# Kernel tuning notes

Measured on AMD Instinct MI355X. Metric: run time of the kernel, lower is better.

The kernel has to match this reference:

```python
import jax, jax.numpy as jnp
import numpy as np

N = 1_048_576      # flattened batch (forward reshapes to (-1, 4))
Q_DIM = 4
HIDDEN = 64
DC = Q_DIM // 2    # q_dim_changed = 2
NUM_LO = (DC * DC - DC) // 2  # = 1
SLOPE = 0.01       # torch leaky_relu default negative slope


def setup_inputs() -> dict:
    key = jax.random.key(0)
    ks = jax.random.split(key, 9)
    def lin(kw, kb, fan_out, fan_in):
        bound = 1.0 / np.sqrt(fan_in)
        W = jax.random.uniform(kw, (fan_out, fan_in), jnp.float32, -bound, bound)
        b = jax.random.uniform(kb, (fan_out,), jnp.float32, -bound, bound)
        return W, b
    x = jax.random.normal(ks[0], (N, Q_DIM), jnp.float32)
    W1, b1 = lin(ks[1], ks[2], HIDDEN, Q_DIM)
    W2, b2 = lin(ks[3], ks[4], HIDDEN, HIDDEN)
    W_Ld, b_Ld = lin(ks[5], ks[6], DC, HIDDEN)
    W_Lo, b_Lo = lin(ks[7], ks[8], NUM_LO, HIDDEN)
    return {"x": x, "W1": W1, "b1": b1, "W2": W2, "b2": b2,
            "W_Ld": W_Ld, "b_Ld": b_Ld, "W_Lo": W_Lo, "b_Lo": b_Lo}


def reference(x, W1, b1, W2, b2, W_Ld, b_Ld, W_Lo, b_Lo):
    q = x.reshape(-1, Q_DIM)                      # (n, 4)
    n = q.shape[0]
    h1 = jax.nn.leaky_relu(q @ W1.T + b1, SLOPE)  # (n, 64)
    h2 = jax.nn.leaky_relu(h1 @ W2.T + b2, SLOPE) # (n, 64); dropout is eval-mode identity
    Ld = jax.nn.softplus(h2 @ W_Ld.T + b_Ld)      # (n, 2) positive diagonal
    Lo = h2 @ W_Lo.T + b_Lo                       # (n, 1) strictly-lower entries
    rows, cols = jnp.tril_indices(DC, -1)         # strictly lower triangle, row-major
    diag = jnp.arange(DC)
    L = jnp.zeros((n, DC, DC), dtype=q.dtype)
    L = L.at[:, rows, cols].set(Lo)               # scatter Lo (matches torch boolean-mask fill order)
    L = L.at[:, diag, diag].set(Ld)               # diag_embed(Ld)
    H = jnp.einsum('nij,nkj->nik', L, L) + 1e-9 * jnp.eye(DC, dtype=q.dtype)
    return H
```

## Files before the change

### kernel.cpp

```cpp
#include <hip/hip_runtime.h>


typedef __attribute__((ext_vector_type(8))) short bf16x8;
typedef __attribute__((ext_vector_type(4))) float f32x4;
typedef __attribute__((ext_vector_type(2))) float f32x2;

#define BLOCK_THREADS 256
#define GRID_BLOCKS   1024

__device__ __forceinline__ float lrelu(float a) {
    return fmaxf(a, 0.01f * a);
}

__device__ __forceinline__ f32x2 lrelu2(f32x2 a) {
    return __builtin_elementwise_max(a, a * 0.01f);
}

__device__ __forceinline__ float softplus(float v) {
    return fmaxf(v, 0.0f) + log1pf(expf(-fabsf(v)));
}

__device__ __forceinline__ unsigned cvt_pk_bf16(float lo, float hi) {
    unsigned r;
    asm("v_cvt_pk_bf16_f32 %0, %1, %2" : "=v"(r) : "v"(lo), "v"(hi));
    return r;
}

__global__ __launch_bounds__(BLOCK_THREADS) void dln_mfma(
    const float* __restrict__ x,
    const float* __restrict__ W1,  const float* __restrict__ b1,
    const float* __restrict__ W2,  const float* __restrict__ b2,
    const float* __restrict__ WLd, const float* __restrict__ bLd,
    const float* __restrict__ WLo, const float* __restrict__ bLo,
    float* __restrict__ out,
    int iters, int iter_stride)
{
    __shared__ __align__(16) unsigned short h1s[4][8][64][8];

    const int tid  = threadIdx.x;
    const int lane = tid & 63;
    const int wv   = tid >> 6;
    const int quad = lane >> 4;
    const int c    = lane & 15;

    int row = blockIdx.x * BLOCK_THREADS + tid;
    float4 qnext = ((const float4*)x)[row];

    bf16x8 afrag[4][2];
    f32x4 wld0[4], wld1[4], wlo[4], b2v[4];
#pragma unroll
    for (int mt = 0; mt < 4; ++mt) {
        const float* wr = W2 + (16 * mt + c) * 64 + 8 * quad;
#pragma unroll
        for (int s = 0; s < 2; ++s) {
            const float4 f0 = *(const float4*)(wr + 32 * s);
            const float4 f1 = *(const float4*)(wr + 32 * s + 4);
            uint4 u;
            u.x = cvt_pk_bf16(f0.x, f0.y);
            u.y = cvt_pk_bf16(f0.z, f0.w);
            u.z = cvt_pk_bf16(f1.x, f1.y);
            u.w = cvt_pk_bf16(f1.z, f1.w);
            afrag[mt][s] = __builtin_bit_cast(bf16x8, u);
        }
        const int nb = 16 * mt + 4 * quad;
        wld0[mt] = *(const f32x4*)(WLd + nb);
        wld1[mt] = *(const f32x4*)(WLd + 64 + nb);
        wlo[mt]  = *(const f32x4*)(WLo + nb);
        b2v[mt]  = *(const f32x4*)(b2 + nb);
    }
    const float bld0 = bLd[0];
    const float bld1 = bLd[1];
    const float blo0 = bLo[0];

    for (int itr = 0; itr < iters; ++itr) {
        const float4 qv = qnext;
        const int row_cur = row;
        row += iter_stride;
        if (itr + 1 < iters)
            qnext = ((const float4*)x)[row];

#pragma unroll
        for (int ch = 0; ch < 8; ++ch) {
            unsigned up[4];
#pragma unroll
            for (int p = 0; p < 4; ++p) {
                float h[2];
#pragma unroll
                for (int e = 0; e < 2; ++e) {
                    const int j = ch * 8 + p * 2 + e;
                    float a = b1[j];
                    a = fmaf(qv.x, W1[4 * j + 0], a);
                    a = fmaf(qv.y, W1[4 * j + 1], a);
                    a = fmaf(qv.z, W1[4 * j + 2], a);
                    a = fmaf(qv.w, W1[4 * j + 3], a);
                    h[e] = lrelu(a);
                }
                up[p] = cvt_pk_bf16(h[0], h[1]);
            }
            *(uint4*)&h1s[wv][ch][lane][0] = make_uint4(up[0], up[1], up[2], up[3]);
        }

        float sld0 = 0.0f, sld1 = 0.0f, slo = 0.0f;
#pragma unroll
        for (int it = 0; it < 4; ++it) {
            const bf16x8 bf0 = *(const bf16x8*)&h1s[wv][quad][it * 16 + c][0];
            const bf16x8 bf1 = *(const bf16x8*)&h1s[wv][4 + quad][it * 16 + c][0];

            f32x2 pld0 = {0.0f, 0.0f}, pld1 = {0.0f, 0.0f}, plo = {0.0f, 0.0f};
#pragma unroll
            for (int mt = 0; mt < 4; ++mt) {
                f32x4 acc = b2v[mt];
                acc = __builtin_amdgcn_mfma_f32_16x16x32_bf16(afrag[mt][0], bf0, acc, 0, 0, 0);
                acc = __builtin_amdgcn_mfma_f32_16x16x32_bf16(afrag[mt][1], bf1, acc, 0, 0, 0);
                const f32x2 hlo = lrelu2((f32x2){acc[0], acc[1]});
                const f32x2 hhi = lrelu2((f32x2){acc[2], acc[3]});
                pld0 = __builtin_elementwise_fma(hlo, (f32x2){wld0[mt][0], wld0[mt][1]}, pld0);
                pld0 = __builtin_elementwise_fma(hhi, (f32x2){wld0[mt][2], wld0[mt][3]}, pld0);
                pld1 = __builtin_elementwise_fma(hlo, (f32x2){wld1[mt][0], wld1[mt][1]}, pld1);
                pld1 = __builtin_elementwise_fma(hhi, (f32x2){wld1[mt][2], wld1[mt][3]}, pld1);
                plo  = __builtin_elementwise_fma(hlo, (f32x2){wlo[mt][0],  wlo[mt][1]},  plo);
                plo  = __builtin_elementwise_fma(hhi, (f32x2){wlo[mt][2],  wlo[mt][3]},  plo);
            }
            float r0 = pld0[0] + pld0[1];
            float r1 = pld1[0] + pld1[1];
            float r2 = plo[0]  + plo[1];
            r0 += __shfl_xor(r0, 16); r0 += __shfl_xor(r0, 32);
            r1 += __shfl_xor(r1, 16); r1 += __shfl_xor(r1, 32);
            r2 += __shfl_xor(r2, 16); r2 += __shfl_xor(r2, 32);
            if (it == quad) { sld0 = r0; sld1 = r1; slo = r2; }
        }

        {
            const float ld0 = softplus(sld0 + bld0);
            const float ld1 = softplus(sld1 + bld1);
            const float lo  = slo + blo0;
            float4 o;
            o.x = fmaf(ld0, ld0, 1e-9f);
            o.y = ld0 * lo;
            o.z = o.y;
            o.w = fmaf(lo, lo, fmaf(ld1, ld1, 1e-9f));
            reinterpret_cast<float4*>(out)[row_cur] = o;
        }
    }
}

__global__ __launch_bounds__(256) void dln_tail(
    const float* __restrict__ x,
    const float* __restrict__ W1,  const float* __restrict__ b1,
    const float* __restrict__ W2,  const float* __restrict__ b2,
    const float* __restrict__ WLd, const float* __restrict__ bLd,
    const float* __restrict__ WLo, const float* __restrict__ bLo,
    float* __restrict__ out, int row0, int nrows)
{
    const int row = row0 + blockIdx.x * 256 + threadIdx.x;
    if (row >= nrows) return;
    const float4 qv = reinterpret_cast<const float4*>(x)[row];
    float h1[64];
#pragma unroll
    for (int j = 0; j < 64; ++j) {
        float a = b1[j];
        a = fmaf(qv.x, W1[4 * j + 0], a);
        a = fmaf(qv.y, W1[4 * j + 1], a);
        a = fmaf(qv.z, W1[4 * j + 2], a);
        a = fmaf(qv.w, W1[4 * j + 3], a);
        h1[j] = lrelu(a);
    }
    float ld0 = bLd[0], ld1 = bLd[1], lo = bLo[0];
#pragma unroll 4
    for (int j = 0; j < 64; ++j) {
        float a0 = b2[j], a1 = 0.0f;
        const float* w = W2 + 64 * j;
#pragma unroll
        for (int k = 0; k < 64; k += 2) {
            a0 = fmaf(h1[k],     w[k],     a0);
            a1 = fmaf(h1[k + 1], w[k + 1], a1);
        }
        const float a = lrelu(a0 + a1);
        ld0 = fmaf(a, WLd[j],      ld0);
        ld1 = fmaf(a, WLd[64 + j], ld1);
        lo  = fmaf(a, WLo[j],      lo);
    }
    ld0 = softplus(ld0);
    ld1 = softplus(ld1);
    float4 o;
    o.x = fmaf(ld0, ld0, 1e-9f);
    o.y = ld0 * lo;
    o.z = o.y;
    o.w = fmaf(lo, lo, fmaf(ld1, ld1, 1e-9f));
    reinterpret_cast<float4*>(out)[row] = o;
}

extern "C" void kernel_launch(void* const* d_in, const int* in_sizes, int n_in,
                              void* d_out, int out_size, void* d_ws, size_t ws_size,
                              hipStream_t stream)
{
    const float* x   = (const float*)d_in[0];
    const float* W1  = (const float*)d_in[1];
    const float* b1  = (const float*)d_in[2];
    const float* W2  = (const float*)d_in[3];
    const float* b2  = (const float*)d_in[4];
    const float* WLd = (const float*)d_in[5];
    const float* bLd = (const float*)d_in[6];
    const float* WLo = (const float*)d_in[7];
    const float* bLo = (const float*)d_in[8];
    float* out = (float*)d_out;

    const int nrows  = in_sizes[0] / 4;
    const int stripe = GRID_BLOCKS * BLOCK_THREADS;
    const int iters  = nrows / stripe;
    const int nfull  = iters * stripe;
    const int rem    = nrows - nfull;

    if (iters > 0)
        dln_mfma<<<GRID_BLOCKS, BLOCK_THREADS, 0, stream>>>(
            x, W1, b1, W2, b2, WLd, bLd, WLo, bLo, out, iters, stripe);
    if (rem > 0)
        dln_tail<<<(rem + 255) / 256, 256, 0, stream>>>(
            x, W1, b1, W2, b2, WLd, bLd, WLo, bLo, out, nfull, nrows);
}
```

Before: 120.6 us.

## Compute first layer with split-bf16 MFMA and drop the LDS staging

Moves the 4→64 first layer from scalar FMAs onto MFMA. W1, the bias and x are split into hi/lo bf16 pairs and three MFMAs per tile recover near-fp32 accuracy, with the bias folded in through a constant-one input column. The layer-1 output now arrives directly in the register layout needed as the B operand of layer 2, so the shared-memory write/read round trip is removed. Row assignment changes to contiguous 256-row groups per block. This cuts VALU work and LDS traffic at the cost of extra MFMA issues, and x is now loaded redundantly across the four quads of each wave.

```diff
diff --git a/kernel.cpp b/kernel.cpp
--- a/kernel.cpp
+++ b/kernel.cpp
@@ -5,8 +5,9 @@
 typedef __attribute__((ext_vector_type(4))) float f32x4;
 typedef __attribute__((ext_vector_type(2))) float f32x2;
 
-#define BLOCK_THREADS 256
-#define GRID_BLOCKS   1024
+#define BLOCK_THREADS  256
+#define GRID_BLOCKS    1024
+#define ROWS_PER_GROUP 256
 
 __device__ __forceinline__ float lrelu(float a) {
     return fmaxf(a, 0.01f * a);
@@ -24,6 +25,11 @@
     unsigned r;
     asm("v_cvt_pk_bf16_f32 %0, %1, %2" : "=v"(r) : "v"(lo), "v"(hi));
     return r;
+}
+
+__device__ __forceinline__ float lo_of(float v, unsigned pk, bool hi_half) {
+    const float h = __uint_as_float(hi_half ? (pk & 0xFFFF0000u) : (pk << 16));
+    return v - h;
 }
 
 __global__ __launch_bounds__(BLOCK_THREADS) void dln_mfma(
@@ -32,19 +38,32 @@
     const float* __restrict__ W2,  const float* __restrict__ b2,
     const float* __restrict__ WLd, const float* __restrict__ bLd,
     const float* __restrict__ WLo, const float* __restrict__ bLo,
-    float* __restrict__ out,
-    int iters, int iter_stride)
+    float* __restrict__ out, int ngroups)
 {
-    __shared__ __align__(16) unsigned short h1s[4][8][64][8];
-
     const int tid  = threadIdx.x;
     const int lane = tid & 63;
     const int wv   = tid >> 6;
     const int quad = lane >> 4;
     const int c    = lane & 15;
 
-    int row = blockIdx.x * BLOCK_THREADS + tid;
-    float4 qnext = ((const float4*)x)[row];
+    bf16x8 a1hi[4], a1lo[4];
+#pragma unroll
+    for (int mt = 0; mt < 4; ++mt) {
+        const int nu = 32 * (mt >> 1) + 8 * (c >> 2) + 4 * (mt & 1) + (c & 3);
+        const float4 w = *(const float4*)(W1 + 4 * nu);
+        const float bb = b1[nu];
+        const unsigned h01 = cvt_pk_bf16(w.x, w.y);
+        const unsigned h23 = cvt_pk_bf16(w.z, w.w);
+        const unsigned hb  = cvt_pk_bf16(bb, 0.0f);
+        const unsigned l01 = cvt_pk_bf16(lo_of(w.x, h01, false), lo_of(w.y, h01, true));
+        const unsigned l23 = cvt_pk_bf16(lo_of(w.z, h23, false), lo_of(w.w, h23, true));
+        const unsigned lb  = cvt_pk_bf16(lo_of(bb, hb, false), 0.0f);
+        const uint4 z  = make_uint4(0u, 0u, 0u, 0u);
+        const uint4 uh = (quad == 0) ? make_uint4(h01, h23, hb, 0u) : z;
+        const uint4 ul = (quad == 0) ? make_uint4(l01, l23, lb, 0u) : z;
+        a1hi[mt] = __builtin_bit_cast(bf16x8, uh);
+        a1lo[mt] = __builtin_bit_cast(bf16x8, ul);
+    }
 
     bf16x8 afrag[4][2];
     f32x4 wld0[4], wld1[4], wlo[4], b2v[4];
@@ -72,39 +91,50 @@
     const float bld1 = bLd[1];
     const float blo0 = bLo[0];
 
-    for (int itr = 0; itr < iters; ++itr) {
-        const float4 qv = qnext;
-        const int row_cur = row;
-        row += iter_stride;
-        if (itr + 1 < iters)
-            qnext = ((const float4*)x)[row];
-
-#pragma unroll
-        for (int ch = 0; ch < 8; ++ch) {
-            unsigned up[4];
-#pragma unroll
-            for (int p = 0; p < 4; ++p) {
-                float h[2];
-#pragma unroll
-                for (int e = 0; e < 2; ++e) {
-                    const int j = ch * 8 + p * 2 + e;
-                    float a = b1[j];
-                    a = fmaf(qv.x, W1[4 * j + 0], a);
-                    a = fmaf(qv.y, W1[4 * j + 1], a);
-                    a = fmaf(qv.z, W1[4 * j + 2], a);
-                    a = fmaf(qv.w, W1[4 * j + 3], a);
-                    h[e] = lrelu(a);
-                }
-                up[p] = cvt_pk_bf16(h[0], h[1]);
+    for (int grp = blockIdx.x; grp < ngroups; grp += gridDim.x) {
+        const int wbase = grp * ROWS_PER_GROUP + wv * 64;
+
+        float4 xv[4];
+#pragma unroll
+        for (int it = 0; it < 4; ++it)
+            xv[it] = ((const float4*)x)[wbase + it * 16 + c];
+
+        float sld0 = 0.0f, sld1 = 0.0f, slo = 0.0f;
+#pragma unroll
+        for (int it = 0; it < 4; ++it) {
+            const unsigned xh01 = cvt_pk_bf16(xv[it].x, xv[it].y);
+            const unsigned xh23 = cvt_pk_bf16(xv[it].z, xv[it].w);
+            const unsigned xl01 = cvt_pk_bf16(lo_of(xv[it].x, xh01, false),
+                                              lo_of(xv[it].y, xh01, true));
+            const unsigned xl23 = cvt_pk_bf16(lo_of(xv[it].z, xh23, false),
+                                              lo_of(xv[it].w, xh23, true));
+            const uint4 z  = make_uint4(0u, 0u, 0u, 0u);
+            const uint4 bh = (quad == 0) ? make_uint4(xh01, xh23, 0x00003F80u, 0u) : z;
+            const uint4 bl = (quad == 0) ? make_uint4(xl01, xl23, 0u, 0u) : z;
+            const bf16x8 bqh = __builtin_bit_cast(bf16x8, bh);
+            const bf16x8 bql = __builtin_bit_cast(bf16x8, bl);
+
+            f32x4 acc1[4];
+#pragma unroll
+            for (int mt = 0; mt < 4; ++mt) {
+                f32x4 a = (f32x4){0.0f, 0.0f, 0.0f, 0.0f};
+                a = __builtin_amdgcn_mfma_f32_16x16x32_bf16(a1hi[mt], bqh, a, 0, 0, 0);
+                a = __builtin_amdgcn_mfma_f32_16x16x32_bf16(a1hi[mt], bql, a, 0, 0, 0);
+                a = __builtin_amdgcn_mfma_f32_16x16x32_bf16(a1lo[mt], bqh, a, 0, 0, 0);
+                acc1[mt] = a;
             }
-            *(uint4*)&h1s[wv][ch][lane][0] = make_uint4(up[0], up[1], up[2], up[3]);
-        }
-
-        float sld0 = 0.0f, sld1 = 0.0f, slo = 0.0f;
-#pragma unroll
-        for (int it = 0; it < 4; ++it) {
-            const bf16x8 bf0 = *(const bf16x8*)&h1s[wv][quad][it * 16 + c][0];
-            const bf16x8 bf1 = *(const bf16x8*)&h1s[wv][4 + quad][it * 16 + c][0];
+
+            uint4 u0, u1;
+            u0.x = cvt_pk_bf16(lrelu(acc1[0][0]), lrelu(acc1[0][1]));
+            u0.y = cvt_pk_bf16(lrelu(acc1[0][2]), lrelu(acc1[0][3]));
+            u0.z = cvt_pk_bf16(lrelu(acc1[1][0]), lrelu(acc1[1][1]));
+            u0.w = cvt_pk_bf16(lrelu(acc1[1][2]), lrelu(acc1[1][3]));
+            u1.x = cvt_pk_bf16(lrelu(acc1[2][0]), lrelu(acc1[2][1]));
+            u1.y = cvt_pk_bf16(lrelu(acc1[2][2]), lrelu(acc1[2][3]));
+            u1.z = cvt_pk_bf16(lrelu(acc1[3][0]), lrelu(acc1[3][1]));
+            u1.w = cvt_pk_bf16(lrelu(acc1[3][2]), lrelu(acc1[3][3]));
+            const bf16x8 bf0 = __builtin_bit_cast(bf16x8, u0);
+            const bf16x8 bf1 = __builtin_bit_cast(bf16x8, u1);
 
             f32x2 pld0 = {0.0f, 0.0f}, pld1 = {0.0f, 0.0f}, plo = {0.0f, 0.0f};
 #pragma unroll
@@ -139,7 +169,7 @@
             o.y = ld0 * lo;
             o.z = o.y;
             o.w = fmaf(lo, lo, fmaf(ld1, ld1, 1e-9f));
-            reinterpret_cast<float4*>(out)[row_cur] = o;
+            reinterpret_cast<float4*>(out)[wbase + lane] = o;
         }
     }
 }
@@ -205,15 +235,16 @@
     const float* bLo = (const float*)d_in[8];
     float* out = (float*)d_out;
 
-    const int nrows  = in_sizes[0] / 4;
-    const int stripe = GRID_BLOCKS * BLOCK_THREADS;
-    const int iters  = nrows / stripe;
-    const int nfull  = iters * stripe;
-    const int rem    = nrows - nfull;
-
-    if (iters > 0)
-        dln_mfma<<<GRID_BLOCKS, BLOCK_THREADS, 0, stream>>>(
-            x, W1, b1, W2, b2, WLd, bLd, WLo, bLo, out, iters, stripe);
+    const int nrows   = in_sizes[0] / 4;
+    const int ngroups = nrows / ROWS_PER_GROUP;
+    const int nfull   = ngroups * ROWS_PER_GROUP;
+    const int rem     = nrows - nfull;
+
+    if (ngroups > 0) {
+        const int grid = (ngroups < GRID_BLOCKS) ? ngroups : GRID_BLOCKS;
+        dln_mfma<<<grid, BLOCK_THREADS, 0, stream>>>(
+            x, W1, b1, W2, b2, WLd, bLd, WLo, bLo, out, ngroups);
+    }
     if (rem > 0)
         dln_tail<<<(rem + 255) / 256, 256, 0, stream>>>(
             x, W1, b1, W2, b2, WLd, bLd, WLo, bLo, out, nfull, nrows);
```

Result: slower. 133.9 us (+11.0%).

## Compute output head with split-bf16 MFMA and permute W2 rows for fragment reuse

Applied to the files above, without the earlier changes.

Replaces the per-lane FMA head projection and cross-lane shuffle reductions with an extra MFMA. Layer-2 activations are repacked into bf16 B-fragments, and W2 rows are permuted so the accumulator layout matches the next MFMA's input. The head weights are split into hi and lo bf16 parts to keep near-fp32 accuracy. The launch also switches to a 1280-block grid-stride loop over 256-row groups. The cost is that layer-2 activations are now rounded to bf16 before the head, which adds precision error.

```diff
diff --git a/kernel.cpp b/kernel.cpp
--- a/kernel.cpp
+++ b/kernel.cpp
@@ -5,8 +5,9 @@
 typedef __attribute__((ext_vector_type(4))) float f32x4;
 typedef __attribute__((ext_vector_type(2))) float f32x2;
 
-#define BLOCK_THREADS 256
-#define GRID_BLOCKS   1024
+#define BLOCK_THREADS  256
+#define GRID_BLOCKS    1280
+#define ROWS_PER_GROUP 256
 
 __device__ __forceinline__ float lrelu(float a) {
     return fmaxf(a, 0.01f * a);
@@ -24,6 +25,11 @@
     unsigned r;
     asm("v_cvt_pk_bf16_f32 %0, %1, %2" : "=v"(r) : "v"(lo), "v"(hi));
     return r;
+}
+
+__device__ __forceinline__ float lo_of(float v, unsigned pk, bool hi_half) {
+    const float h = __uint_as_float(hi_half ? (pk & 0xFFFF0000u) : (pk << 16));
+    return v - h;
 }
 
 __global__ __launch_bounds__(BLOCK_THREADS) void dln_mfma(
@@ -32,8 +38,7 @@
     const float* __restrict__ W2,  const float* __restrict__ b2,
     const float* __restrict__ WLd, const float* __restrict__ bLd,
     const float* __restrict__ WLo, const float* __restrict__ bLo,
-    float* __restrict__ out,
-    int iters, int iter_stride)
+    float* __restrict__ out, int ngroups)
 {
     __shared__ __align__(16) unsigned short h1s[4][8][64][8];
 
@@ -43,14 +48,15 @@
     const int quad = lane >> 4;
     const int c    = lane & 15;
 
-    int row = blockIdx.x * BLOCK_THREADS + tid;
-    float4 qnext = ((const float4*)x)[row];
+    int grp = blockIdx.x;
+    float4 qnext = ((const float4*)x)[grp * ROWS_PER_GROUP + tid];
 
     bf16x8 afrag[4][2];
-    f32x4 wld0[4], wld1[4], wlo[4], b2v[4];
+    f32x4 b2v[4];
 #pragma unroll
     for (int mt = 0; mt < 4; ++mt) {
-        const float* wr = W2 + (16 * mt + c) * 64 + 8 * quad;
+        const int nu = 32 * (mt >> 1) + 8 * (c >> 2) + 4 * (mt & 1) + (c & 3);
+        const float* wr = W2 + nu * 64 + 8 * quad;
 #pragma unroll
         for (int s = 0; s < 2; ++s) {
             const float4 f0 = *(const float4*)(wr + 32 * s);
@@ -62,22 +68,45 @@
             u.w = cvt_pk_bf16(f1.z, f1.w);
             afrag[mt][s] = __builtin_bit_cast(bf16x8, u);
         }
-        const int nb = 16 * mt + 4 * quad;
-        wld0[mt] = *(const f32x4*)(WLd + nb);
-        wld1[mt] = *(const f32x4*)(WLd + 64 + nb);
-        wlo[mt]  = *(const f32x4*)(WLo + nb);
-        b2v[mt]  = *(const f32x4*)(b2 + nb);
+        b2v[mt] = *(const f32x4*)(b2 + 32 * (mt >> 1) + 4 * (mt & 1) + 8 * quad);
+    }
+
+    bf16x8 hA[2][2];
+    {
+        const float* hw = (c == 0) ? WLd : (c == 1) ? (WLd + 64) : WLo;
+#pragma unroll
+        for (int s = 0; s < 2; ++s) {
+            uint4 uh = make_uint4(0u, 0u, 0u, 0u);
+            uint4 ul = make_uint4(0u, 0u, 0u, 0u);
+            if (c < 3) {
+                const float* p = hw + 32 * s + 8 * quad;
+                const float4 f0 = *(const float4*)(p);
+                const float4 f1 = *(const float4*)(p + 4);
+                uh.x = cvt_pk_bf16(f0.x, f0.y);
+                uh.y = cvt_pk_bf16(f0.z, f0.w);
+                uh.z = cvt_pk_bf16(f1.x, f1.y);
+                uh.w = cvt_pk_bf16(f1.z, f1.w);
+                ul.x = cvt_pk_bf16(lo_of(f0.x, uh.x, false), lo_of(f0.y, uh.x, true));
+                ul.y = cvt_pk_bf16(lo_of(f0.z, uh.y, false), lo_of(f0.w, uh.y, true));
+                ul.z = cvt_pk_bf16(lo_of(f1.x, uh.z, false), lo_of(f1.y, uh.z, true));
+                ul.w = cvt_pk_bf16(lo_of(f1.z, uh.w, false), lo_of(f1.w, uh.w, true));
+            }
+            hA[s][0] = __builtin_bit_cast(bf16x8, uh);
+            hA[s][1] = __builtin_bit_cast(bf16x8, ul);
+        }
     }
     const float bld0 = bLd[0];
     const float bld1 = bLd[1];
     const float blo0 = bLo[0];
-
-    for (int itr = 0; itr < iters; ++itr) {
+    const f32x4 hinit = (quad == 0) ? (f32x4){bld0, bld1, blo0, 0.0f}
+                                    : (f32x4){0.0f, 0.0f, 0.0f, 0.0f};
+
+    for (; grp < ngroups; grp += (int)gridDim.x) {
         const float4 qv = qnext;
-        const int row_cur = row;
-        row += iter_stride;
-        if (itr + 1 < iters)
-            qnext = ((const float4*)x)[row];
+        const int gn = grp + (int)gridDim.x;
+        if (gn < ngroups)
+            qnext = ((const float4*)x)[gn * ROWS_PER_GROUP + tid];
+        const int wbase = grp * ROWS_PER_GROUP + wv * 64;
 
 #pragma unroll
         for (int ch = 0; ch < 8; ++ch) {
@@ -100,13 +129,12 @@
             *(uint4*)&h1s[wv][ch][lane][0] = make_uint4(up[0], up[1], up[2], up[3]);
         }
 
-        float sld0 = 0.0f, sld1 = 0.0f, slo = 0.0f;
 #pragma unroll
         for (int it = 0; it < 4; ++it) {
             const bf16x8 bf0 = *(const bf16x8*)&h1s[wv][quad][it * 16 + c][0];
             const bf16x8 bf1 = *(const bf16x8*)&h1s[wv][4 + quad][it * 16 + c][0];
 
-            f32x2 pld0 = {0.0f, 0.0f}, pld1 = {0.0f, 0.0f}, plo = {0.0f, 0.0f};
+            uint4 u0, u1;
 #pragma unroll
             for (int mt = 0; mt < 4; ++mt) {
                 f32x4 acc = b2v[mt];
@@ -114,32 +142,33 @@
                 acc = __builtin_amdgcn_mfma_f32_16x16x32_bf16(afrag[mt][1], bf1, acc, 0, 0, 0);
                 const f32x2 hlo = lrelu2((f32x2){acc[0], acc[1]});
                 const f32x2 hhi = lrelu2((f32x2){acc[2], acc[3]});
-                pld0 = __builtin_elementwise_fma(hlo, (f32x2){wld0[mt][0], wld0[mt][1]}, pld0);
-                pld0 = __builtin_elementwise_fma(hhi, (f32x2){wld0[mt][2], wld0[mt][3]}, pld0);
-                pld1 = __builtin_elementwise_fma(hlo, (f32x2){wld1[mt][0], wld1[mt][1]}, pld1);
-                pld1 = __builtin_elementwise_fma(hhi, (f32x2){wld1[mt][2], wld1[mt][3]}, pld1);
-                plo  = __builtin_elementwise_fma(hlo, (f32x2){wlo[mt][0],  wlo[mt][1]},  plo);
-                plo  = __builtin_elementwise_fma(hhi, (f32x2){wlo[mt][2],  wlo[mt][3]},  plo);
-            }
-            float r0 = pld0[0] + pld0[1];
-            float r1 = pld1[0] + pld1[1];
-            float r2 = plo[0]  + plo[1];
-            r0 += __shfl_xor(r0, 16); r0 += __shfl_xor(r0, 32);
-            r1 += __shfl_xor(r1, 16); r1 += __shfl_xor(r1, 32);
-            r2 += __shfl_xor(r2, 16); r2 += __shfl_xor(r2, 32);
-            if (it == quad) { sld0 = r0; sld1 = r1; slo = r2; }
-        }
-
-        {
-            const float ld0 = softplus(sld0 + bld0);
-            const float ld1 = softplus(sld1 + bld1);
-            const float lo  = slo + blo0;
-            float4 o;
-            o.x = fmaf(ld0, ld0, 1e-9f);
-            o.y = ld0 * lo;
-            o.z = o.y;
-            o.w = fmaf(lo, lo, fmaf(ld1, ld1, 1e-9f));
-            reinterpret_cast<float4*>(out)[row_cur] = o;
+                const unsigned pa = cvt_pk_bf16(hlo[0], hlo[1]);
+                const unsigned pb = cvt_pk_bf16(hhi[0], hhi[1]);
+                if (mt == 0)      { u0.x = pa; u0.y = pb; }
+                else if (mt == 1) { u0.z = pa; u0.w = pb; }
+                else if (mt == 2) { u1.x = pa; u1.y = pb; }
+                else              { u1.z = pa; u1.w = pb; }
+            }
+            const bf16x8 bh0 = __builtin_bit_cast(bf16x8, u0);
+            const bf16x8 bh1 = __builtin_bit_cast(bf16x8, u1);
+
+            f32x4 hacc = hinit;
+            hacc = __builtin_amdgcn_mfma_f32_16x16x32_bf16(hA[0][0], bh0, hacc, 0, 0, 0);
+            hacc = __builtin_amdgcn_mfma_f32_16x16x32_bf16(hA[0][1], bh0, hacc, 0, 0, 0);
+            hacc = __builtin_amdgcn_mfma_f32_16x16x32_bf16(hA[1][0], bh1, hacc, 0, 0, 0);
+            hacc = __builtin_amdgcn_mfma_f32_16x16x32_bf16(hA[1][1], bh1, hacc, 0, 0, 0);
+
+            if (quad == 0) {
+                const float ld0 = softplus(hacc[0]);
+                const float ld1 = softplus(hacc[1]);
+                const float lo  = hacc[2];
+                float4 o;
+                o.x = fmaf(ld0, ld0, 1e-9f);
+                o.y = ld0 * lo;
+                o.z = o.y;
+                o.w = fmaf(lo, lo, fmaf(ld1, ld1, 1e-9f));
+                reinterpret_cast<float4*>(out)[wbase + it * 16 + c] = o;
+            }
         }
     }
 }
@@ -205,15 +234,16 @@
     const float* bLo = (const float*)d_in[8];
     float* out = (float*)d_out;
 
-    const int nrows  = in_sizes[0] / 4;
-    const int stripe = GRID_BLOCKS * BLOCK_THREADS;
-    const int iters  = nrows / stripe;
-    const int nfull  = iters * stripe;
-    const int rem    = nrows - nfull;
-
-    if (iters > 0)
-        dln_mfma<<<GRID_BLOCKS, BLOCK_THREADS, 0, stream>>>(
-            x, W1, b1, W2, b2, WLd, bLd, WLo, bLo, out, iters, stripe);
+    const int nrows   = in_sizes[0] / 4;
+    const int ngroups = nrows / ROWS_PER_GROUP;
+    const int nfull   = ngroups * ROWS_PER_GROUP;
+    const int rem     = nrows - nfull;
+
+    if (ngroups > 0) {
+        const int grid = (ngroups < GRID_BLOCKS) ? ngroups : GRID_BLOCKS;
+        dln_mfma<<<grid, BLOCK_THREADS, 0, stream>>>(
+            x, W1, b1, W2, b2, WLd, bLd, WLo, bLo, out, ngroups);
+    }
     if (rem > 0)
         dln_tail<<<(rem + 255) / 256, 256, 0, stream>>>(
             x, W1, b1, W2, b2, WLd, bLd, WLo, bLo, out, nfull, nrows);
```

After: 137.5 us. 1.14x slower.

## Software-pipeline layer-1 compute with MFMA layer-2 via double-buffered LDS

Applied to the files above, without the earlier changes.

Restructures the main loop so the layer-1 activations for the next row batch are computed and written into one LDS buffer while MFMA layer-2 work reads the other buffer, interleaving the VALU and MFMA phases. It also halves the block size and doubles the grid so that the double-buffered shared memory per block stays the same size. The goal is to overlap the VALU-bound first layer with matrix-core work. The cost is more register pressure from the extra in-flight state and a peeled final iteration. It relies on each wave touching only its own LDS slice, so no barriers are needed.

```diff
diff --git a/kernel.cpp b/kernel.cpp
--- a/kernel.cpp
+++ b/kernel.cpp
@@ -5,8 +5,8 @@
 typedef __attribute__((ext_vector_type(4))) float f32x4;
 typedef __attribute__((ext_vector_type(2))) float f32x2;
 
-#define BLOCK_THREADS 256
-#define GRID_BLOCKS   1024
+#define BLOCK_THREADS 128
+#define GRID_BLOCKS   2048
 
 __device__ __forceinline__ float lrelu(float a) {
     return fmaxf(a, 0.01f * a);
@@ -35,7 +35,7 @@
     float* __restrict__ out,
     int iters, int iter_stride)
 {
-    __shared__ __align__(16) unsigned short h1s[4][8][64][8];
+    __shared__ __align__(16) unsigned short h1s[2][2][8][64][8];
 
     const int tid  = threadIdx.x;
     const int lane = tid & 63;
@@ -44,7 +44,7 @@
     const int c    = lane & 15;
 
     int row = blockIdx.x * BLOCK_THREADS + tid;
-    float4 qnext = ((const float4*)x)[row];
+    const float4 q0 = ((const float4*)x)[row];
 
     bf16x8 afrag[4][2];
     f32x4 wld0[4], wld1[4], wlo[4], b2v[4];
@@ -72,75 +72,95 @@
     const float bld1 = bLd[1];
     const float blo0 = bLo[0];
 
-    for (int itr = 0; itr < iters; ++itr) {
-        const float4 qv = qnext;
+    auto P1 = [&](int wbuf, const float4& qv, int ch) {
+        unsigned up[4];
+#pragma unroll
+        for (int p = 0; p < 4; ++p) {
+            float h[2];
+#pragma unroll
+            for (int e = 0; e < 2; ++e) {
+                const int j = ch * 8 + p * 2 + e;
+                float a = b1[j];
+                a = fmaf(qv.x, W1[4 * j + 0], a);
+                a = fmaf(qv.y, W1[4 * j + 1], a);
+                a = fmaf(qv.z, W1[4 * j + 2], a);
+                a = fmaf(qv.w, W1[4 * j + 3], a);
+                h[e] = lrelu(a);
+            }
+            up[p] = cvt_pk_bf16(h[0], h[1]);
+        }
+        *(uint4*)&h1s[wbuf][wv][ch][lane][0] = make_uint4(up[0], up[1], up[2], up[3]);
+    };
+
+    auto P2IT = [&](int rbuf, int it, float& d0, float& d1, float& d2) {
+        const bf16x8 bf0 = *(const bf16x8*)&h1s[rbuf][wv][quad][it * 16 + c][0];
+        const bf16x8 bf1 = *(const bf16x8*)&h1s[rbuf][wv][4 + quad][it * 16 + c][0];
+        f32x2 pld0 = {0.0f, 0.0f}, pld1 = {0.0f, 0.0f}, plo = {0.0f, 0.0f};
+#pragma unroll
+        for (int mt = 0; mt < 4; ++mt) {
+            f32x4 acc = b2v[mt];
+            acc = __builtin_amdgcn_mfma_f32_16x16x32_bf16(afrag[mt][0], bf0, acc, 0, 0, 0);
+            acc = __builtin_amdgcn_mfma_f32_16x16x32_bf16(afrag[mt][1], bf1, acc, 0, 0, 0);
+            const f32x2 hlo = lrelu2((f32x2){acc[0], acc[1]});
+            const f32x2 hhi = lrelu2((f32x2){acc[2], acc[3]});
+            pld0 = __builtin_elementwise_fma(hlo, (f32x2){wld0[mt][0], wld0[mt][1]}, pld0);
+            pld0 = __builtin_elementwise_fma(hhi, (f32x2){wld0[mt][2], wld0[mt][3]}, pld0);
+            pld1 = __builtin_elementwise_fma(hlo, (f32x2){wld1[mt][0], wld1[mt][1]}, pld1);
+            pld1 = __builtin_elementwise_fma(hhi, (f32x2){wld1[mt][2], wld1[mt][3]}, pld1);
+            plo  = __builtin_elementwise_fma(hlo, (f32x2){wlo[mt][0],  wlo[mt][1]},  plo);
+            plo  = __builtin_elementwise_fma(hhi, (f32x2){wlo[mt][2],  wlo[mt][3]},  plo);
+        }
+        float r0 = pld0[0] + pld0[1];
+        float r1 = pld1[0] + pld1[1];
+        float r2 = plo[0]  + plo[1];
+        r0 += __shfl_xor(r0, 16); r0 += __shfl_xor(r0, 32);
+        r1 += __shfl_xor(r1, 16); r1 += __shfl_xor(r1, 32);
+        r2 += __shfl_xor(r2, 16); r2 += __shfl_xor(r2, 32);
+        if (it == quad) { d0 = r0; d1 = r1; d2 = r2; }
+    };
+
+    auto EPI = [&](int row_out, float sld0, float sld1, float slo) {
+        const float ld0 = softplus(sld0 + bld0);
+        const float ld1 = softplus(sld1 + bld1);
+        const float lo  = slo + blo0;
+        float4 o;
+        o.x = fmaf(ld0, ld0, 1e-9f);
+        o.y = ld0 * lo;
+        o.z = o.y;
+        o.w = fmaf(lo, lo, fmaf(ld1, ld1, 1e-9f));
+        reinterpret_cast<float4*>(out)[row_out] = o;
+    };
+
+#pragma unroll
+    for (int ch = 0; ch < 8; ++ch) P1(0, q0, ch);
+    float4 qnext = ((const float4*)x)[(iters > 1) ? row + iter_stride : row];
+
+    for (int itr = 0; itr < iters - 1; ++itr) {
+        const float4 qp1 = qnext;
         const int row_cur = row;
         row += iter_stride;
-        if (itr + 1 < iters)
-            qnext = ((const float4*)x)[row];
-
-#pragma unroll
-        for (int ch = 0; ch < 8; ++ch) {
-            unsigned up[4];
-#pragma unroll
-            for (int p = 0; p < 4; ++p) {
-                float h[2];
-#pragma unroll
-                for (int e = 0; e < 2; ++e) {
-                    const int j = ch * 8 + p * 2 + e;
-                    float a = b1[j];
-                    a = fmaf(qv.x, W1[4 * j + 0], a);
-                    a = fmaf(qv.y, W1[4 * j + 1], a);
-                    a = fmaf(qv.z, W1[4 * j + 2], a);
-                    a = fmaf(qv.w, W1[4 * j + 3], a);
-                    h[e] = lrelu(a);
-                }
-                up[p] = cvt_pk_bf16(h[0], h[1]);
-            }
-            *(uint4*)&h1s[wv][ch][lane][0] = make_uint4(up[0], up[1], up[2], up[3]);
-        }
+        const int rload = (itr + 2 < iters) ? row + iter_stride : row;
+        qnext = ((const float4*)x)[rload];
+        const int rbuf = itr & 1;
+        const int wbuf = rbuf ^ 1;
 
         float sld0 = 0.0f, sld1 = 0.0f, slo = 0.0f;
-#pragma unroll
-        for (int it = 0; it < 4; ++it) {
-            const bf16x8 bf0 = *(const bf16x8*)&h1s[wv][quad][it * 16 + c][0];
-            const bf16x8 bf1 = *(const bf16x8*)&h1s[wv][4 + quad][it * 16 + c][0];
-
-            f32x2 pld0 = {0.0f, 0.0f}, pld1 = {0.0f, 0.0f}, plo = {0.0f, 0.0f};
-#pragma unroll
-            for (int mt = 0; mt < 4; ++mt) {
-                f32x4 acc = b2v[mt];
-                acc = __builtin_amdgcn_mfma_f32_16x16x32_bf16(afrag[mt][0], bf0, acc, 0, 0, 0);
-                acc = __builtin_amdgcn_mfma_f32_16x16x32_bf16(afrag[mt][1], bf1, acc, 0, 0, 0);
-                const f32x2 hlo = lrelu2((f32x2){acc[0], acc[1]});
-                const f32x2 hhi = lrelu2((f32x2){acc[2], acc[3]});
-                pld0 = __builtin_elementwise_fma(hlo, (f32x2){wld0[mt][0], wld0[mt][1]}, pld0);
-                pld0 = __builtin_elementwise_fma(hhi, (f32x2){wld0[mt][2], wld0[mt][3]}, pld0);
-                pld1 = __builtin_elementwise_fma(hlo, (f32x2){wld1[mt][0], wld1[mt][1]}, pld1);
-                pld1 = __builtin_elementwise_fma(hhi, (f32x2){wld1[mt][2], wld1[mt][3]}, pld1);
-                plo  = __builtin_elementwise_fma(hlo, (f32x2){wlo[mt][0],  wlo[mt][1]},  plo);
-                plo  = __builtin_elementwise_fma(hhi, (f32x2){wlo[mt][2],  wlo[mt][3]},  plo);
-            }
-            float r0 = pld0[0] + pld0[1];
-            float r1 = pld1[0] + pld1[1];
-            float r2 = plo[0]  + plo[1];
-            r0 += __shfl_xor(r0, 16); r0 += __shfl_xor(r0, 32);
-            r1 += __shfl_xor(r1, 16); r1 += __shfl_xor(r1, 32);
-            r2 += __shfl_xor(r2, 16); r2 += __shfl_xor(r2, 32);
-            if (it == quad) { sld0 = r0; sld1 = r1; slo = r2; }
-        }
-
-        {
-            const float ld0 = softplus(sld0 + bld0);
-            const float ld1 = softplus(sld1 + bld1);
-            const float lo  = slo + blo0;
-            float4 o;
-            o.x = fmaf(ld0, ld0, 1e-9f);
-            o.y = ld0 * lo;
-            o.z = o.y;
-            o.w = fmaf(lo, lo, fmaf(ld1, ld1, 1e-9f));
-            reinterpret_cast<float4*>(out)[row_cur] = o;
-        }
+        P1(wbuf, qp1, 0); P1(wbuf, qp1, 1); P2IT(rbuf, 0, sld0, sld1, slo);
+        P1(wbuf, qp1, 2); P1(wbuf, qp1, 3); P2IT(rbuf, 1, sld0, sld1, slo);
+        P1(wbuf, qp1, 4); P1(wbuf, qp1, 5); P2IT(rbuf, 2, sld0, sld1, slo);
+        P1(wbuf, qp1, 6); P1(wbuf, qp1, 7); P2IT(rbuf, 3, sld0, sld1, slo);
+
+        EPI(row_cur, sld0, sld1, slo);
+    }
+
+    {
+        const int rbuf = (iters - 1) & 1;
+        float sld0 = 0.0f, sld1 = 0.0f, slo = 0.0f;
+        P2IT(rbuf, 0, sld0, sld1, slo);
+        P2IT(rbuf, 1, sld0, sld1, slo);
+        P2IT(rbuf, 2, sld0, sld1, slo);
+        P2IT(rbuf, 3, sld0, sld1, slo);
+        EPI(row, sld0, sld1, slo);
     }
 }
 
```

New measurement: 131.1 us. 8.7% more time.
